# Kernel tuning notes

Hardware: AMD Instinct MI355X
Metric: run time of the kernel (lower is better)

## Reference

```python
import jax, jax.numpy as jnp
import numpy as np

B, S, D = 2, 2048, 1024
H, DK = 16, 64          # heads, d_k (= d_v)
DH = 4096               # FFN hidden
EPS = 1e-5


def _layer_norm(x, gamma, beta):
    mu = jnp.mean(x, axis=-1, keepdims=True)
    var = jnp.var(x, axis=-1, keepdims=True)
    return (x - mu) * jax.lax.rsqrt(var + EPS) * gamma + beta


def setup_inputs() -> dict:
    key = jax.random.key(0)
    ks = jax.random.split(key, 8)
    s = lambda fan_in: 1.0 / np.sqrt(fan_in)
    return {
        "x": jax.random.normal(ks[0], (B, S, D), dtype=jnp.float32),
        # NOTE: source module uses W_q for queries, keys AND values (bug kept faithfully),
        # so W_k / W_v are never used and are not materialized.
        "Wq": jax.random.normal(ks[1], (D, H * DK), dtype=jnp.float32) * s(D),
        "bq": jnp.zeros((H * DK,), dtype=jnp.float32),
        "Wo": jax.random.normal(ks[2], (H * DK, D), dtype=jnp.float32) * s(H * DK),
        "bo": jnp.zeros((D,), dtype=jnp.float32),
        "ln1_g": jnp.ones((D,), dtype=jnp.float32),
        "ln1_b": jnp.zeros((D,), dtype=jnp.float32),
        "W1": jax.random.normal(ks[3], (D, DH), dtype=jnp.float32) * s(D),
        "b1": jnp.zeros((DH,), dtype=jnp.float32),
        "W2": jax.random.normal(ks[4], (DH, D), dtype=jnp.float32) * s(DH),
        "b2": jnp.zeros((D,), dtype=jnp.float32),
        "ln2_g": jnp.ones((D,), dtype=jnp.float32),
        "ln2_b": jnp.zeros((D,), dtype=jnp.float32),
    }


def reference(x, Wq, bq, Wo, bo, ln1_g, ln1_b, W1, b1, W2, b2, ln2_g, ln2_b):
    residual = x
    # projections: q, k, v all use W_q (faithful to source)
    q = (x @ Wq + bq).reshape(B, S, H, DK)
    k = (x @ Wq + bq).reshape(B, S, H, DK)
    v = (x @ Wq + bq).reshape(B, S, H, DK)
    # scores scaled by sqrt(sequence_length), as in the source
    scale = 1.0 / jnp.sqrt(jnp.float32(S))
    scores = jnp.einsum("bqhd,bkhd->bhqk", q, k) * scale
    probs = jax.nn.softmax(scores, axis=-1)
    attn = jnp.einsum("bhqk,bkhd->bqhd", probs, v).reshape(B, S, H * DK)
    attn = attn @ Wo + bo
    # dropout is identity in eval mode
    x = _layer_norm(attn + residual, ln1_g, ln1_b)
    residual = x
    h = jax.nn.relu(x @ W1 + b1)
    x = h @ W2 + b2
    x = _layer_norm(x + residual, ln2_g, ln2_b)
    return x
```

## Files before the change

### kernel.cpp

```cpp
#include <hip/hip_runtime.h>
#include <stdint.h>


typedef unsigned short u16;
typedef __attribute__((ext_vector_type(8))) short v8s;
typedef __attribute__((ext_vector_type(4))) float v4f;

#define AS1 __attribute__((address_space(1)))
#define AS3 __attribute__((address_space(3)))

__device__ __forceinline__ void gl_lds16(const u16* g, u16* l) {
  __builtin_amdgcn_global_load_lds((const AS1 void*)g, (AS3 void*)l, 16, 0, 0);
}

__device__ __forceinline__ float bf2f(u16 u) {
  union { uint32_t i; float f; } v; v.i = ((uint32_t)u) << 16; return v.f;
}
__device__ __forceinline__ u16 f2bf(float f) {
  union { float f; uint32_t i; } v; v.f = f;
  uint32_t x = v.i;
  return (u16)((x + 0x7FFFu + ((x >> 16) & 1u)) >> 16);
}
__device__ __forceinline__ uint32_t fbits(float f) {
  union { float f; uint32_t u; } v; v.f = f; return v.u;
}

__global__ __launch_bounds__(256) void cvt_f2b(
    const float* __restrict__ src, u16* __restrict__ dst, int n4) {
  int i = (blockIdx.x * 256 + threadIdx.x);
  if (i < n4) {
    float4 v = *(const float4*)(src + (size_t)i * 4);
    ushort4 o;
    o.x = f2bf(v.x); o.y = f2bf(v.y); o.z = f2bf(v.z); o.w = f2bf(v.w);
    *(ushort4*)(dst + (size_t)i * 4) = o;
  }
}

__global__ __launch_bounds__(256) void transpose_f2b(
    const float* __restrict__ src, u16* __restrict__ dst,
    int R, int C, int ld_s, int ld_d) {
  __shared__ float tile[32][33];
  const int tx = threadIdx.x & 31, ty = threadIdx.x >> 5;
  const int c0 = blockIdx.x * 32, r0 = blockIdx.y * 32;
#pragma unroll
  for (int j = 0; j < 32; j += 8)
    tile[ty + j][tx] = src[(size_t)(r0 + ty + j) * ld_s + c0 + tx];
  __syncthreads();
#pragma unroll
  for (int j = 0; j < 32; j += 8)
    dst[(size_t)(c0 + ty + j) * ld_d + r0 + tx] = f2bf(tile[tx][ty + j]);
}

__global__ __launch_bounds__(256) void transpose_b2b(
    const u16* __restrict__ src, u16* __restrict__ dst,
    int R, int C, int ld_s, int ld_d) {
  __shared__ u16 tile[32][33];
  const int tx = threadIdx.x & 31, ty = threadIdx.x >> 5;
  const int c0 = blockIdx.x * 32, r0 = blockIdx.y * 32;
#pragma unroll
  for (int j = 0; j < 32; j += 8)
    tile[ty + j][tx] = src[(size_t)(r0 + ty + j) * ld_s + c0 + tx];
  __syncthreads();
#pragma unroll
  for (int j = 0; j < 32; j += 8)
    dst[(size_t)(c0 + ty + j) * ld_d + r0 + tx] = tile[tx][ty + j];
}

__global__ __launch_bounds__(512, 1) void gemm_8p(
    const u16* __restrict__ A, const u16* __restrict__ Bt,
    const float* __restrict__ bias, void* __restrict__ C0,
    u16* __restrict__ C1, u16* __restrict__ C2, u16* __restrict__ C3,
    int M, int N, int ldk, int klen, int relu, int c0_f32) {
  __shared__ u16 As[2][16384];
  __shared__ u16 Bs[2][16384];
  const int tid = threadIdx.x;
  const int w = tid >> 6, l = tid & 63;
  const int l16 = l & 15, kgrp = (l >> 4) & 3;
  const int wm = w >> 2, wn = w & 3;
  const int m0 = blockIdx.y * 256, n0 = blockIdx.x * 256;
  const int z = blockIdx.z;
  const int NT = klen >> 6;

  const int rl = tid >> 3;
  const int sw = 8 * ((tid & 7) ^ (rl & 7));
  const u16* gA[4]; const u16* gB[4];
#pragma unroll
  for (int j = 0; j < 4; j++) {
    gA[j] = A + (size_t)(m0 + j * 64 + rl) * ldk + (size_t)z * klen + sw;
    gB[j] = Bt + (size_t)(n0 + j * 64 + rl) * ldk + (size_t)z * klen + sw;
  }
  const int sdst = w * 512;

  const int ch0 = 8 * ((kgrp) ^ (l16 & 7));
  const int ch1 = 8 * ((4 + kgrp) ^ (l16 & 7));
  const int abase = (wm * 128 + l16) * 64;
  const int bbase = (wn * 64 + l16) * 64;

  v4f acc[8][4];
#pragma unroll
  for (int i = 0; i < 8; i++)
#pragma unroll
    for (int j = 0; j < 4; j++)
#pragma unroll
      for (int r = 0; r < 4; r++) acc[i][j][r] = 0.f;

  v8s a[4][2], b[4][2];

#define FENCE() asm volatile("" ::: "memory")
#define VMC(n) asm volatile("s_waitcnt vmcnt(" #n ")" ::: "memory")
#define BARX() { __builtin_amdgcn_s_barrier(); \
                 __builtin_amdgcn_sched_barrier(0); FENCE(); }
#define STGA(q, j, kt) gl_lds16(gA[j] + (size_t)(kt) * 64, &As[q][(j) * 4096 + sdst])
#define STGB(q, j, kt) gl_lds16(gB[j] + (size_t)(kt) * 64, &Bs[q][(j) * 4096 + sdst])
#define LDA(p, mh) { \
  const u16* Ap = &As[p][abase + (mh) * 4096]; \
  _Pragma("unroll") for (int mi = 0; mi < 4; mi++) { \
    a[mi][0] = *(const v8s*)(Ap + mi * 1024 + ch0); \
    a[mi][1] = *(const v8s*)(Ap + mi * 1024 + ch1); } }
#define LDB(p, nh) { \
  const u16* Bp = &Bs[p][bbase + (nh) * 2048]; \
  _Pragma("unroll") for (int ni = 0; ni < 2; ni++) { \
    b[(nh) * 2 + ni][0] = *(const v8s*)(Bp + ni * 1024 + ch0); \
    b[(nh) * 2 + ni][1] = *(const v8s*)(Bp + ni * 1024 + ch1); } }
#define MFQ(mh, nh) { \
  __builtin_amdgcn_s_setprio(1); \
  _Pragma("unroll") for (int ks = 0; ks < 2; ks++) \
  _Pragma("unroll") for (int mi = 0; mi < 4; mi++) \
  _Pragma("unroll") for (int ni = 0; ni < 2; ni++) \
    acc[(mh) * 4 + mi][(nh) * 2 + ni] = __builtin_amdgcn_mfma_f32_16x16x32_bf16( \
        a[mi][ks], b[(nh) * 2 + ni][ks], acc[(mh) * 4 + mi][(nh) * 2 + ni], 0, 0, 0); \
  __builtin_amdgcn_s_setprio(0); }

  STGA(0, 0, 0); STGA(0, 2, 0);
  FENCE();
  STGB(0, 0, 0); STGB(0, 1, 0);
  FENCE();
  STGB(0, 2, 0); STGB(0, 3, 0);
  FENCE();
  STGA(0, 1, 0); STGA(0, 3, 0);
  VMC(2); BARX();

  int p = 0;
  for (int kt = 0; kt < NT - 1; ++kt, p ^= 1) {
    const int q = p ^ 1;
    const int kn = kt + 1;
    LDA(p, 0);
    LDB(p, 0);
    FENCE();
    STGA(q, 0, kn); STGA(q, 2, kn);
    MFQ(0, 0);
    LDB(p, 1);
    FENCE();
    STGB(q, 0, kn); STGB(q, 1, kn);
    VMC(4); BARX();
    MFQ(0, 1);
    LDA(p, 1);
    FENCE();
    STGB(q, 2, kn); STGB(q, 3, kn);
    MFQ(1, 1);
    FENCE();
    STGA(q, 1, kn); STGA(q, 3, kn);
    VMC(2); BARX();
    MFQ(1, 0);
  }
  VMC(0); BARX();
  LDA(p, 0);
  LDB(p, 0);
  MFQ(0, 0);
  LDB(p, 1);
  MFQ(0, 1);
  LDA(p, 1);
  MFQ(1, 1);
  MFQ(1, 0);

#undef FENCE
#undef VMC
#undef BARX
#undef STGA
#undef STGB
#undef LDA
#undef LDB
#undef MFQ

#pragma unroll
  for (int mi = 0; mi < 8; mi++) {
    const int row = m0 + wm * 128 + mi * 16 + kgrp * 4;
#pragma unroll
    for (int ni = 0; ni < 4; ni++) {
      const int col = n0 + wn * 64 + ni * 16 + l16;
      float bv = (bias && z == 0) ? bias[col] : 0.f;
#pragma unroll
      for (int r = 0; r < 4; r++) {
        float v = acc[mi][ni][r] + bv;
        if (z == 0 && relu) v = fmaxf(v, 0.f);
        size_t idx = (size_t)(row + r) * N + col;
        if (z == 0) {
          if (c0_f32) ((float*)C0)[idx] = v;
          else ((u16*)C0)[idx] = f2bf(v);
        } else if (z == 1) {
          C1[idx] = f2bf(v);
        } else if (z == 2) {
          C2[idx] = f2bf(v);
        } else {
          C3[idx] = f2bf(v);
        }
      }
    }
  }
}

__global__ __launch_bounds__(256) void gemm_g2(
    const u16* __restrict__ A, const u16* __restrict__ Bt,
    const float* __restrict__ bias, void* __restrict__ C,
    int M, int N, int K, int relu, int accum, int out_f32) {
  __shared__ u16 As[2][8192];
  __shared__ u16 Bs[2][4096];
  const int tid = threadIdx.x;
  const int w = tid >> 6, l = tid & 63;
  const int l16 = l & 15, kgrp = l >> 4;
  const int m0 = blockIdx.y * 128, n0 = blockIdx.x * 64;
  const int wr = (w >> 1) * 64, wc = (w & 1) * 32;

  const int srow = w * 8 + (l >> 3);
  const u16* gA[4];
#pragma unroll
  for (int i = 0; i < 4; i++) {
    int r = i * 32 + srow;
    gA[i] = A + (size_t)(m0 + r) * K + 8 * ((l & 7) ^ (r & 7));
  }
  const u16* gB[2];
#pragma unroll
  for (int i = 0; i < 2; i++) {
    int r = i * 32 + srow;
    gB[i] = Bt + (size_t)(n0 + r) * K + 8 * ((l & 7) ^ (r & 7));
  }

  v4f acc[4][2];
#pragma unroll
  for (int i = 0; i < 4; i++)
#pragma unroll
    for (int j = 0; j < 2; j++)
#pragma unroll
      for (int r = 0; r < 4; r++) acc[i][j][r] = 0.f;

#pragma unroll
  for (int i = 0; i < 4; i++) gl_lds16(gA[i], &As[0][(i * 256 + w * 64) * 8]);
#pragma unroll
  for (int i = 0; i < 2; i++) gl_lds16(gB[i], &Bs[0][(i * 256 + w * 64) * 8]);

  int cur = 0;
  for (int k0 = 0; k0 < K; k0 += 64) {
    __syncthreads();
    if (k0 + 64 < K) {
      int nxt = cur ^ 1;
#pragma unroll
      for (int i = 0; i < 4; i++)
        gl_lds16(gA[i] + k0 + 64, &As[nxt][(i * 256 + w * 64) * 8]);
#pragma unroll
      for (int i = 0; i < 2; i++)
        gl_lds16(gB[i] + k0 + 64, &Bs[nxt][(i * 256 + w * 64) * 8]);
    }
    v8s a[4][2], b[2][2];
#pragma unroll
    for (int ks = 0; ks < 2; ks++) {
      int ch = 8 * ((ks * 4 + kgrp) ^ (l16 & 7));
#pragma unroll
      for (int mi = 0; mi < 4; mi++)
        a[mi][ks] = *(const v8s*)(&As[cur][(wr + mi * 16 + l16) * 64 + ch]);
#pragma unroll
      for (int ni = 0; ni < 2; ni++)
        b[ni][ks] = *(const v8s*)(&Bs[cur][(wc + ni * 16 + l16) * 64 + ch]);
    }
#pragma unroll
    for (int ks = 0; ks < 2; ks++)
#pragma unroll
      for (int mi = 0; mi < 4; mi++)
#pragma unroll
        for (int ni = 0; ni < 2; ni++)
          acc[mi][ni] = __builtin_amdgcn_mfma_f32_16x16x32_bf16(a[mi][ks], b[ni][ks], acc[mi][ni], 0, 0, 0);
    cur ^= 1;
  }

#pragma unroll
  for (int ni = 0; ni < 2; ni++) {
    int col = n0 + wc + ni * 16 + l16;
    float bv = bias ? bias[col] : 0.f;
#pragma unroll
    for (int mi = 0; mi < 4; mi++) {
      int row = m0 + wr + mi * 16 + kgrp * 4;
#pragma unroll
      for (int r = 0; r < 4; r++) {
        float v = acc[mi][ni][r] + bv;
        if (relu) v = fmaxf(v, 0.f);
        size_t idx = (size_t)(row + r) * N + col;
        if (out_f32) {
          float* Cf = (float*)C;
          if (accum) v += Cf[idx];
          Cf[idx] = v;
        } else {
          ((u16*)C)[idx] = f2bf(v);
        }
      }
    }
  }
}

__global__ __launch_bounds__(512) void attn_kernel(
    const u16* __restrict__ Q, const u16* __restrict__ Qt,
    u16* __restrict__ O) {
  __shared__ u16 KV[2][8192];
  __shared__ __align__(16) u16 Ps[8][1152];
  const int tid = threadIdx.x;
  const int w = tid >> 6, l = tid & 63;
  const int l16 = l & 15, kgrp = l >> 4;
  const int bh = blockIdx.y, b = bh >> 4, h = bh & 15;
  const int q0 = blockIdx.x * 128;
  const size_t rowQ = (size_t)(b * 2048 + q0 + w * 16);
  const float cexp = 1.4426950408889634f / 45.254833995939045f;

  const int isV = w >> 2, wl = w & 3;
  const int r0 = wl * 16 + (l >> 3);
  const int sch8 = 8 * ((l & 7) ^ (l >> 3));
  const u16* gS0;
  size_t kstep;
  if (!isV) {
    gS0 = Q + (size_t)(b * 2048 + r0) * 1024 + h * 64 + sch8;
    kstep = 1024;
  } else {
    gS0 = Qt + (size_t)(h * 64 + r0) * 4096 + b * 2048 + sch8;
    kstep = 1;
  }
  const u16* gS1 = gS0 + (size_t)8 * (isV ? 4096 : 1024);
  const int ldst = isV * 4096 + wl * 1024;

  v8s qb[2];
#pragma unroll
  for (int ks = 0; ks < 2; ks++) {
    v8s t = *(const v8s*)(Q + (rowQ + l16) * 1024 + h * 64 + ks * 32 + kgrp * 8);
#pragma unroll
    for (int j = 0; j < 8; j++) t[j] = (short)f2bf(bf2f((u16)t[j]) * cexp);
    qb[ks] = t;
  }

  v4f o[4];
  float ls = 0.f;
#pragma unroll
  for (int j = 0; j < 4; j++)
#pragma unroll
    for (int r = 0; r < 4; r++) o[j][r] = 0.f;

  gl_lds16(gS0, &KV[0][ldst]);
  gl_lds16(gS1, &KV[0][ldst + 512]);

  u16* Pw = &Ps[w][0];
  int cur = 0;
  for (int kb = 0; kb < 2048; kb += 64) {
    __syncthreads();
    if (kb + 64 < 2048) {
      int nxt = cur ^ 1;
      gl_lds16(gS0 + (size_t)(kb + 64) * kstep, &KV[nxt][ldst]);
      gl_lds16(gS1 + (size_t)(kb + 64) * kstep, &KV[nxt][ldst + 512]);
    }
    const u16* Ks = &KV[cur][0];
    const u16* Vt = &KV[cur][4096];

    v4f st[4];
#pragma unroll
    for (int i = 0; i < 4; i++)
#pragma unroll
      for (int r = 0; r < 4; r++) st[i][r] = 0.f;
#pragma unroll
    for (int ks = 0; ks < 2; ks++) {
      v8s ka[4];
#pragma unroll
      for (int mi = 0; mi < 4; mi++)
        ka[mi] = *(const v8s*)(Ks + (mi * 16 + l16) * 64 + 8 * ((ks * 4 + kgrp) ^ (l16 & 7)));
#pragma unroll
      for (int mi = 0; mi < 4; mi++)
        st[mi] = __builtin_amdgcn_mfma_f32_16x16x32_bf16(ka[mi], qb[ks], st[mi], 0, 0, 0);
    }

#pragma unroll
    for (int mi = 0; mi < 4; mi++) {
      float p0 = __builtin_amdgcn_exp2f(st[mi][0]);
      float p1 = __builtin_amdgcn_exp2f(st[mi][1]);
      float p2 = __builtin_amdgcn_exp2f(st[mi][2]);
      float p3 = __builtin_amdgcn_exp2f(st[mi][3]);
      ls += (p0 + p1) + (p2 + p3);
      uint2 pk;
      pk.x = __builtin_amdgcn_perm(fbits(p1), fbits(p0), 0x07060302u);
      pk.y = __builtin_amdgcn_perm(fbits(p3), fbits(p2), 0x07060302u);
      *(uint2*)(Pw + l16 * 72 + mi * 16 + kgrp * 4) = pk;
    }

#pragma unroll
    for (int t = 0; t < 2; t++) {
      v8s pa, vb[4];
      pa = *(const v8s*)(Pw + l16 * 72 + t * 32 + kgrp * 8);
#pragma unroll
      for (int ni = 0; ni < 4; ni++)
        vb[ni] = *(const v8s*)(Vt + (ni * 16 + l16) * 64 + 8 * ((t * 4 + kgrp) ^ (l16 & 7)));
#pragma unroll
      for (int ni = 0; ni < 4; ni++)
        o[ni] = __builtin_amdgcn_mfma_f32_16x16x32_bf16(pa, vb[ni], o[ni], 0, 0, 0);
    }
    cur ^= 1;
  }

  {
    float t = ls;
    t += __shfl_xor(t, 16, 64);
    t += __shfl_xor(t, 32, 64);
    ls = t;
  }

#pragma unroll
  for (int r = 0; r < 4; r++) {
    float den = __shfl(ls, kgrp * 4 + r, 64);
    float rden = 1.f / den;
#pragma unroll
    for (int ni = 0; ni < 4; ni++) {
      O[(rowQ + kgrp * 4 + r) * 1024 + h * 64 + ni * 16 + l16] =
          f2bf(o[ni][r] * rden);
    }
  }
}

__global__ __launch_bounds__(256) void ln_residual(
    const void* __restrict__ Y, const void* __restrict__ Y2,
    const void* __restrict__ Y3, const void* __restrict__ Y4,
    const void* __restrict__ Xr,
    const float* __restrict__ g, const float* __restrict__ bb,
    void* __restrict__ out, int yf, int y2f, int xf, int of) {
  const int row = blockIdx.x, tid = threadIdx.x;
  const size_t base = (size_t)row * 1024;
  float v[4], s = 0.f, sq = 0.f;
#pragma unroll
  for (int i = 0; i < 4; i++) {
    int c = tid + i * 256;
    float ya = yf ? ((const float*)Y)[base + c] : bf2f(((const u16*)Y)[base + c]);
    float xa = xf ? ((const float*)Xr)[base + c] : bf2f(((const u16*)Xr)[base + c]);
    float x = ya + xa;
    if (Y2) {
      float y2a = y2f ? ((const float*)Y2)[base + c] : bf2f(((const u16*)Y2)[base + c]);
      x += y2a;
    }
    if (Y3) x += bf2f(((const u16*)Y3)[base + c]);
    if (Y4) x += bf2f(((const u16*)Y4)[base + c]);
    v[i] = x; s += x; sq += x * x;
  }
#pragma unroll
  for (int off = 32; off >= 1; off >>= 1) {
    s += __shfl_down(s, off, 64);
    sq += __shfl_down(sq, off, 64);
  }
  __shared__ float rs[4], rq[4];
  const int w = tid >> 6, l = tid & 63;
  if (l == 0) { rs[w] = s; rq[w] = sq; }
  __syncthreads();
  s = rs[0] + rs[1] + rs[2] + rs[3];
  sq = rq[0] + rq[1] + rq[2] + rq[3];
  const float mu = s * (1.f / 1024.f);
  const float var = sq * (1.f / 1024.f) - mu * mu;
  const float rstd = rsqrtf(var + 1e-5f);
#pragma unroll
  for (int i = 0; i < 4; i++) {
    int c = tid + i * 256;
    float r = (v[i] - mu) * rstd * g[c] + bb[c];
    if (of) ((float*)out)[base + c] = r;
    else ((u16*)out)[base + c] = f2bf(r);
  }
}

extern "C" void kernel_launch(void* const* d_in, const int* in_sizes, int n_in,
                              void* d_out, int out_size, void* d_ws, size_t ws_size,
                              hipStream_t stream) {
  const float* x   = (const float*)d_in[0];
  const float* Wq  = (const float*)d_in[1];
  const float* bq  = (const float*)d_in[2];
  const float* Wo  = (const float*)d_in[3];
  const float* bo  = (const float*)d_in[4];
  const float* g1  = (const float*)d_in[5];
  const float* be1 = (const float*)d_in[6];
  const float* W1  = (const float*)d_in[7];
  const float* b1  = (const float*)d_in[8];
  const float* W2  = (const float*)d_in[9];
  const float* b2  = (const float*)d_in[10];
  const float* g2  = (const float*)d_in[11];
  const float* be2 = (const float*)d_in[12];
  float* out = (float*)d_out;
  u16* ws  = (u16*)d_ws;

  const size_t M1 = 1048576;
  dim3 blk(256);
  dim3 blk8(512);
  const bool big = ws_size >= (size_t)37 * M1 * 2;

  if (big) {
    u16* xb   = ws + 0;
    u16* Qb   = ws + 4 * M1;
    u16* Qt   = ws + 8 * M1;
    u16* WqT  = ws + 12 * M1;
    u16* W1T  = ws + 13 * M1;
    u16* W2T  = ws + 17 * M1;
    u16* Hh   = ws + 21 * M1;
    u16* attn = xb;  u16* Yb = Qt;  u16* x1 = Qb;  u16* WoT = WqT;
    u16* P1wo = W1T;
    u16* P2wo = W2T;
    u16* P3wo = Hh;
    u16* P1f2 = Qt;
    u16* P2f2 = xb;
    u16* P3f2 = W1T;

    cvt_f2b<<<dim3(4096), blk, 0, stream>>>(x, xb, 1048576);
    transpose_f2b<<<dim3(32, 32), blk, 0, stream>>>(Wq, WqT, 1024, 1024, 1024, 1024);
    gemm_g2<<<dim3(16, 32), blk, 0, stream>>>(xb, WqT, bq, Qb, 4096, 1024, 1024, 0, 0, 0);

    transpose_b2b<<<dim3(32, 128), blk, 0, stream>>>(Qb, Qt, 4096, 1024, 1024, 4096);
    attn_kernel<<<dim3(16, 32), blk8, 0, stream>>>(Qb, Qt, attn);

    transpose_f2b<<<dim3(32, 32), blk, 0, stream>>>(Wo, WoT, 1024, 1024, 1024, 1024);
    gemm_8p<<<dim3(4, 16, 4), blk8, 0, stream>>>(attn, WoT, bo, Yb, P1wo, P2wo, P3wo,
                                                 4096, 1024, 1024, 256, 0, 0);
    ln_residual<<<dim3(4096), blk, 0, stream>>>(Yb, P1wo, P2wo, P3wo, x, g1, be1, x1,
                                                0, 0, 1, 0);

    transpose_f2b<<<dim3(128, 32), blk, 0, stream>>>(W1, W1T, 1024, 4096, 4096, 1024);
    gemm_8p<<<dim3(16, 16, 1), blk8, 0, stream>>>(x1, W1T, b1, Hh,
                                                  nullptr, nullptr, nullptr,
                                                  4096, 4096, 1024, 1024, 1, 0);

    transpose_f2b<<<dim3(32, 128), blk, 0, stream>>>(W2, W2T, 4096, 1024, 1024, 4096);
    gemm_8p<<<dim3(4, 16, 4), blk8, 0, stream>>>(Hh, W2T, b2, out, P1f2, P2f2, P3f2,
                                                 4096, 1024, 4096, 1024, 0, 1);

    ln_residual<<<dim3(4096), blk, 0, stream>>>(out, P1f2, P2f2, P3f2, x1, g2, be2, out,
                                                1, 0, 0, 1);
  } else {
    u16* xb   = ws + 0;
    u16* Qb   = ws + 4 * M1;
    u16* Qt   = ws + 8 * M1;
    u16* attn = xb;  u16* Yb = Qt;  u16* x1 = Qb;  u16* Hc = xb;
    u16* Wt1  = ws + 12 * M1;
    u16* Wt2  = ws + 13 * M1;

    cvt_f2b<<<dim3(4096), blk, 0, stream>>>(x, xb, 1048576);
    transpose_f2b<<<dim3(32, 32), blk, 0, stream>>>(Wq, Wt1, 1024, 1024, 1024, 1024);
    gemm_g2<<<dim3(16, 32), blk, 0, stream>>>(xb, Wt1, bq, Qb, 4096, 1024, 1024, 0, 0, 0);

    transpose_b2b<<<dim3(32, 128), blk, 0, stream>>>(Qb, Qt, 4096, 1024, 1024, 4096);
    attn_kernel<<<dim3(16, 32), blk8, 0, stream>>>(Qb, Qt, attn);

    transpose_f2b<<<dim3(32, 32), blk, 0, stream>>>(Wo, Wt2, 1024, 1024, 1024, 1024);
    gemm_g2<<<dim3(16, 32), blk, 0, stream>>>(attn, Wt2, bo, Yb, 4096, 1024, 1024, 0, 0, 0);
    ln_residual<<<dim3(4096), blk, 0, stream>>>(Yb, nullptr, nullptr, nullptr, x, g1, be1,
                                                x1, 0, 0, 1, 0);

    for (int c = 0; c < 4; c++) {
      transpose_f2b<<<dim3(32, 32), blk, 0, stream>>>(W1 + (size_t)c * 1024, Wt1,
                                                      1024, 1024, 4096, 1024);
      gemm_g2<<<dim3(16, 32), blk, 0, stream>>>(x1, Wt1, b1 + (size_t)c * 1024, Hc,
                                                4096, 1024, 1024, 1, 0, 0);
      transpose_f2b<<<dim3(32, 32), blk, 0, stream>>>(W2 + (size_t)c * M1, Wt2,
                                                      1024, 1024, 1024, 1024);
      gemm_g2<<<dim3(16, 32), blk, 0, stream>>>(Hc, Wt2, (c == 0) ? b2 : (const float*)nullptr,
                                                out, 4096, 1024, 1024, 0, (c > 0) ? 1 : 0, 1);
    }
    ln_residual<<<dim3(4096), blk, 0, stream>>>(out, nullptr, nullptr, nullptr, x1, g2, be2,
                                                out, 1, 0, 0, 1);
  }
}
```

Measured before the change: 341.7 us.

## Switch attention to 32x32 MFMA with in-register P via permlane32 swap

Rewrites the attention kernel to use 32x32x16 bf16 MFMA tiles, so each wave handles 32 query rows and each block 256 rows (grid halved). The P matrix is no longer round-tripped through shared memory: softmax probabilities are packed to bf16 and rearranged across lane halves with permlane32_swap to form the A operand of the PV MFMA. This targets LDS traffic and per-tile K/V reuse, since each K/V tile loaded into LDS now serves twice as many queries. In exchange it raises register pressure (two 16-float accumulators for scores and two for outputs) and halves the block count, which may lower occupancy and load balance.

Result: no change. 339.8 us (-0.6%).

```diff
diff --git a/kernel.cpp b/kernel.cpp
--- a/kernel.cpp
+++ b/kernel.cpp
@@ -5,6 +5,8 @@
 typedef unsigned short u16;
 typedef __attribute__((ext_vector_type(8))) short v8s;
 typedef __attribute__((ext_vector_type(4))) float v4f;
+typedef __attribute__((ext_vector_type(16))) float v16f;
+typedef __attribute__((ext_vector_type(2))) unsigned int v2u;
 
 #define AS1 __attribute__((address_space(1)))
 #define AS3 __attribute__((address_space(3)))
@@ -309,13 +311,12 @@
     const u16* __restrict__ Q, const u16* __restrict__ Qt,
     u16* __restrict__ O) {
   __shared__ u16 KV[2][8192];
-  __shared__ __align__(16) u16 Ps[8][1152];
   const int tid = threadIdx.x;
   const int w = tid >> 6, l = tid & 63;
-  const int l16 = l & 15, kgrp = l >> 4;
+  const int l31 = l & 31, hi = l >> 5;
   const int bh = blockIdx.y, b = bh >> 4, h = bh & 15;
-  const int q0 = blockIdx.x * 128;
-  const size_t rowQ = (size_t)(b * 2048 + q0 + w * 16);
+  const int q0 = blockIdx.x * 256;
+  const size_t rowQ = (size_t)(b * 2048 + q0 + w * 32);
   const float cexp = 1.4426950408889634f / 45.254833995939045f;
 
   const int isV = w >> 2, wl = w & 3;
@@ -333,26 +334,23 @@
   const u16* gS1 = gS0 + (size_t)8 * (isV ? 4096 : 1024);
   const int ldst = isV * 4096 + wl * 1024;
 
-  v8s qb[2];
-#pragma unroll
-  for (int ks = 0; ks < 2; ks++) {
-    v8s t = *(const v8s*)(Q + (rowQ + l16) * 1024 + h * 64 + ks * 32 + kgrp * 8);
-#pragma unroll
-    for (int j = 0; j < 8; j++) t[j] = (short)f2bf(bf2f((u16)t[j]) * cexp);
-    qb[ks] = t;
-  }
-
-  v4f o[4];
+  v8s qb[4];
+#pragma unroll
+  for (int t = 0; t < 4; t++) {
+    v8s v = *(const v8s*)(Q + (rowQ + l31) * 1024 + h * 64 + t * 16 + hi * 8);
+#pragma unroll
+    for (int j = 0; j < 8; j++) v[j] = (short)f2bf(bf2f((u16)v[j]) * cexp);
+    qb[t] = v;
+  }
+
+  v16f o0, o1;
+#pragma unroll
+  for (int r = 0; r < 16; r++) { o0[r] = 0.f; o1[r] = 0.f; }
   float ls = 0.f;
-#pragma unroll
-  for (int j = 0; j < 4; j++)
-#pragma unroll
-    for (int r = 0; r < 4; r++) o[j][r] = 0.f;
 
   gl_lds16(gS0, &KV[0][ldst]);
   gl_lds16(gS1, &KV[0][ldst + 512]);
 
-  u16* Pw = &Ps[w][0];
   int cur = 0;
   for (int kb = 0; kb < 2048; kb += 64) {
     __syncthreads();
@@ -364,65 +362,59 @@
     const u16* Ks = &KV[cur][0];
     const u16* Vt = &KV[cur][4096];
 
-    v4f st[4];
-#pragma unroll
-    for (int i = 0; i < 4; i++)
-#pragma unroll
-      for (int r = 0; r < 4; r++) st[i][r] = 0.f;
-#pragma unroll
-    for (int ks = 0; ks < 2; ks++) {
-      v8s ka[4];
-#pragma unroll
-      for (int mi = 0; mi < 4; mi++)
-        ka[mi] = *(const v8s*)(Ks + (mi * 16 + l16) * 64 + 8 * ((ks * 4 + kgrp) ^ (l16 & 7)));
-#pragma unroll
-      for (int mi = 0; mi < 4; mi++)
-        st[mi] = __builtin_amdgcn_mfma_f32_16x16x32_bf16(ka[mi], qb[ks], st[mi], 0, 0, 0);
-    }
-
-#pragma unroll
-    for (int mi = 0; mi < 4; mi++) {
-      float p0 = __builtin_amdgcn_exp2f(st[mi][0]);
-      float p1 = __builtin_amdgcn_exp2f(st[mi][1]);
-      float p2 = __builtin_amdgcn_exp2f(st[mi][2]);
-      float p3 = __builtin_amdgcn_exp2f(st[mi][3]);
-      ls += (p0 + p1) + (p2 + p3);
-      uint2 pk;
-      pk.x = __builtin_amdgcn_perm(fbits(p1), fbits(p0), 0x07060302u);
-      pk.y = __builtin_amdgcn_perm(fbits(p3), fbits(p2), 0x07060302u);
-      *(uint2*)(Pw + l16 * 72 + mi * 16 + kgrp * 4) = pk;
-    }
-
-#pragma unroll
-    for (int t = 0; t < 2; t++) {
-      v8s pa, vb[4];
-      pa = *(const v8s*)(Pw + l16 * 72 + t * 32 + kgrp * 8);
-#pragma unroll
-      for (int ni = 0; ni < 4; ni++)
-        vb[ni] = *(const v8s*)(Vt + (ni * 16 + l16) * 64 + 8 * ((t * 4 + kgrp) ^ (l16 & 7)));
-#pragma unroll
-      for (int ni = 0; ni < 4; ni++)
-        o[ni] = __builtin_amdgcn_mfma_f32_16x16x32_bf16(pa, vb[ni], o[ni], 0, 0, 0);
-    }
+    v16f s0, s1;
+#pragma unroll
+    for (int r = 0; r < 16; r++) { s0[r] = 0.f; s1[r] = 0.f; }
+#pragma unroll
+    for (int t = 0; t < 4; t++) {
+      const int c = 8 * ((2 * t + hi) ^ (l & 7));
+      v8s ka0 = *(const v8s*)(Ks + l31 * 64 + c);
+      v8s ka1 = *(const v8s*)(Ks + (32 + l31) * 64 + c);
+      s0 = __builtin_amdgcn_mfma_f32_32x32x16_bf16(ka0, qb[t], s0, 0, 0, 0);
+      s1 = __builtin_amdgcn_mfma_f32_32x32x16_bf16(ka1, qb[t], s1, 0, 0, 0);
+    }
+
+    float p0[16], p1[16];
+#pragma unroll
+    for (int r = 0; r < 16; r++) {
+      p0[r] = __builtin_amdgcn_exp2f(s0[r]);
+      p1[r] = __builtin_amdgcn_exp2f(s1[r]);
+      ls += p0[r] + p1[r];
+    }
+
+#define PVSTEP(t, P) { \
+      const int off = 8 * ((t) & 1); \
+      uint32_t dw00 = __builtin_amdgcn_perm(fbits(P[off + 1]), fbits(P[off + 0]), 0x07060302u); \
+      uint32_t dw01 = __builtin_amdgcn_perm(fbits(P[off + 3]), fbits(P[off + 2]), 0x07060302u); \
+      uint32_t dw10 = __builtin_amdgcn_perm(fbits(P[off + 5]), fbits(P[off + 4]), 0x07060302u); \
+      uint32_t dw11 = __builtin_amdgcn_perm(fbits(P[off + 7]), fbits(P[off + 6]), 0x07060302u); \
+      v2u sA = __builtin_amdgcn_permlane32_swap(dw00, dw10, false, false); \
+      v2u sB = __builtin_amdgcn_permlane32_swap(dw01, dw11, false, false); \
+      union { uint32_t u[4]; v8s v; } pa; \
+      pa.u[0] = sA[0]; pa.u[1] = sB[0]; pa.u[2] = sA[1]; pa.u[3] = sB[1]; \
+      const int c = 8 * ((2 * (t) + hi) ^ (l & 7)); \
+      v8s vb0 = *(const v8s*)(Vt + l31 * 64 + c); \
+      v8s vb1 = *(const v8s*)(Vt + (32 + l31) * 64 + c); \
+      o0 = __builtin_amdgcn_mfma_f32_32x32x16_bf16(pa.v, vb0, o0, 0, 0, 0); \
+      o1 = __builtin_amdgcn_mfma_f32_32x32x16_bf16(pa.v, vb1, o1, 0, 0, 0); }
+    PVSTEP(0, p0)
+    PVSTEP(1, p0)
+    PVSTEP(2, p1)
+    PVSTEP(3, p1)
+#undef PVSTEP
     cur ^= 1;
   }
 
-  {
-    float t = ls;
-    t += __shfl_xor(t, 16, 64);
-    t += __shfl_xor(t, 32, 64);
-    ls = t;
-  }
-
-#pragma unroll
-  for (int r = 0; r < 4; r++) {
-    float den = __shfl(ls, kgrp * 4 + r, 64);
+  ls += __shfl_xor(ls, 32, 64);
+
+  const int hiq = hi * 4;
+#pragma unroll
+  for (int r = 0; r < 16; r++) {
+    const int qo = (r & 3) + 8 * (r >> 2) + hiq;
+    float den = __shfl(ls, qo, 64);
     float rden = 1.f / den;
-#pragma unroll
-    for (int ni = 0; ni < 4; ni++) {
-      O[(rowQ + kgrp * 4 + r) * 1024 + h * 64 + ni * 16 + l16] =
-          f2bf(o[ni][r] * rden);
-    }
+    O[(rowQ + qo) * 1024 + h * 64 + l31] = f2bf(o0[r] * rden);
+    O[(rowQ + qo) * 1024 + h * 64 + 32 + l31] = f2bf(o1[r] * rden);
   }
 }
 
@@ -517,7 +509,7 @@
     gemm_g2<<<dim3(16, 32), blk, 0, stream>>>(xb, WqT, bq, Qb, 4096, 1024, 1024, 0, 0, 0);
 
     transpose_b2b<<<dim3(32, 128), blk, 0, stream>>>(Qb, Qt, 4096, 1024, 1024, 4096);
-    attn_kernel<<<dim3(16, 32), blk8, 0, stream>>>(Qb, Qt, attn);
+    attn_kernel<<<dim3(8, 32), blk8, 0, stream>>>(Qb, Qt, attn);
 
     transpose_f2b<<<dim3(32, 32), blk, 0, stream>>>(Wo, WoT, 1024, 1024, 1024, 1024);
     gemm_8p<<<dim3(4, 16, 4), blk8, 0, stream>>>(attn, WoT, bo, Yb, P1wo, P2wo, P3wo,
@@ -549,7 +541,7 @@
     gemm_g2<<<dim3(16, 32), blk, 0, stream>>>(xb, Wt1, bq, Qb, 4096, 1024, 1024, 0, 0, 0);
 
     transpose_b2b<<<dim3(32, 128), blk, 0, stream>>>(Qb, Qt, 4096, 1024, 1024, 4096);
-    attn_kernel<<<dim3(16, 32), blk8, 0, stream>>>(Qb, Qt, attn);
+    attn_kernel<<<dim3(8, 32), blk8, 0, stream>>>(Qb, Qt, attn);
 
     transpose_f2b<<<dim3(32, 32), blk, 0, stream>>>(Wo, Wt2, 1024, 1024, 1024, 1024);
     gemm_g2<<<dim3(16, 32), blk, 0, stream>>>(attn, Wt2, bo, Yb, 4096, 1024, 1024, 0, 0, 0);
```
